# Kernel optimization log

Hardware: AMD Instinct MI355X
Metric: run time of the kernel (lower is better)

## Reference

```python
import jax, jax.numpy as jnp
import numpy as np

NUM_HEADS = 16

def setup_inputs() -> dict:
    key = jax.random.key(0)
    k1, k2, k3 = jax.random.split(key, 3)
    B, S, H = 2, 2048, 1024
    x = jax.random.normal(k1, (B, S, H), dtype=jnp.float32)
    w_qkv = jax.random.normal(k2, (H, 3 * H), dtype=jnp.float32) * (1.0 / np.sqrt(H))
    w_out = jax.random.normal(k3, (H, H), dtype=jnp.float32) * (1.0 / np.sqrt(H))
    return {"x": x, "w_qkv": w_qkv, "w_out": w_out}

def reference(x, w_qkv, w_out):
    B, S, H = x.shape
    nh = NUM_HEADS
    dh = H // nh
    qkv = x @ w_qkv  # (B, S, 3H)
    q, k, v = jnp.split(qkv, 3, axis=-1)
    # (B, nh, S, dh)
    q = q.reshape(B, S, nh, dh).transpose(0, 2, 1, 3)
    k = k.reshape(B, S, nh, dh).transpose(0, 2, 1, 3)
    v = v.reshape(B, S, nh, dh).transpose(0, 2, 1, 3)
    att = jnp.einsum('bhsd,bhSd->bhsS', q, k) / np.sqrt(dh).astype(np.float32)
    causal = jnp.tril(jnp.ones((S, S), dtype=bool))
    att = jnp.where(causal[None, None], att, -jnp.inf)
    att = jax.nn.softmax(att, axis=-1)
    out = jnp.einsum('bhsS,bhSd->bhsd', att, v)
    out = out.transpose(0, 2, 1, 3).reshape(B, S, H)
    return out @ w_out
```

## Files before the change

kernel.cpp:

```cpp
#include <hip/hip_runtime.h>

#define DEVINL __device__ __forceinline__

typedef __attribute__((ext_vector_type(8)))  __bf16         bf16x8;
typedef __attribute__((ext_vector_type(4)))  float          f32x4;
typedef __attribute__((ext_vector_type(16))) float          f32x16;
typedef __attribute__((ext_vector_type(8)))  unsigned short ushort8;
typedef __attribute__((ext_vector_type(4)))  unsigned short ushort4v;
typedef __attribute__((ext_vector_type(4)))  unsigned int   uint4v;
typedef __attribute__((ext_vector_type(4)))  float          float4v;

DEVINL unsigned short f2bf(float f) {
  unsigned int u = __float_as_uint(f);
  u += 0x7fffu + ((u >> 16) & 1u);
  return (unsigned short)(u >> 16);
}

DEVINL float bf2f(unsigned short u) {
  return __uint_as_float(((unsigned int)u) << 16);
}

DEVINL bf16x8 ldbf8(const unsigned short* p) {
  return __builtin_bit_cast(bf16x8, *(const ushort8*)p);
}

DEVINL unsigned cvtpk_bf16(float lo, float hi) {
  unsigned r;
  asm("v_cvt_pk_bf16_f32 %0, %1, %2" : "=v"(r) : "v"(lo), "v"(hi));
  return r;
}

DEVINL void gload_lds16(const unsigned short* g, unsigned short* l) {
  __builtin_amdgcn_global_load_lds((const __attribute__((address_space(1))) void*)g,
                                   (__attribute__((address_space(3))) void*)l, 16, 0, 0);
}

__global__ __launch_bounds__(256) void cvt_f32_bf16_kernel(
    const float* __restrict__ in, unsigned short* __restrict__ out, int n4) {
  int i = blockIdx.x * 256 + threadIdx.x;
  const int stride = gridDim.x * 256;
  for (; i < n4; i += stride) {
    float4v v = *(const float4v*)(in + (size_t)4 * i);
    ushort4v o;
    o[0] = f2bf(v[0]); o[1] = f2bf(v[1]); o[2] = f2bf(v[2]); o[3] = f2bf(v[3]);
    *(ushort4v*)(out + (size_t)4 * i) = o;
  }
}

__global__ __launch_bounds__(256) void transpose_cvt_kernel(
    const float* __restrict__ in, unsigned short* __restrict__ out, int R, int C) {
  __shared__ float tile[32][33];
  const int tx = threadIdx.x & 31, ty = threadIdx.x >> 5;
  const int r0 = blockIdx.y << 5, c0 = blockIdx.x << 5;
#pragma unroll
  for (int i = 0; i < 32; i += 8)
    tile[ty + i][tx] = in[(size_t)(r0 + ty + i) * C + (c0 + tx)];
  __syncthreads();
#pragma unroll
  for (int i = 0; i < 32; i += 8)
    out[(size_t)(c0 + ty + i) * R + (r0 + tx)] = f2bf(tile[tx][ty + i]);
}

template <bool OUT_BF16>
__global__ __launch_bounds__(256, 3) void gemm_bt_kernel(
    const unsigned short* __restrict__ A,
    const unsigned short* __restrict__ Bt,
    void* __restrict__ Cout,
    int M, int N, int K, int lda, int ldb, int ldc,
    unsigned short* __restrict__ VtOut) {
  __shared__ __align__(16) unsigned short As[2][128 * 32];
  __shared__ __align__(16) unsigned short Bs[2][128 * 32];
  const int tid = threadIdx.x;
  const int lane = tid & 63, wave = tid >> 6;
  const int wr = wave >> 1, wc = wave & 1;
  const int g = lane >> 4, q = lane & 15;
  const int row0 = blockIdx.x << 7, col0 = blockIdx.y << 7;

  const int srow = tid >> 2;
  const int sg = ((tid & 3) ^ (srow & 3)) << 3;
  const unsigned short* Ap0 = A + (size_t)(row0 + srow) * lda + sg;
  const unsigned short* Ap1 = Ap0 + (size_t)64 * lda;
  const unsigned short* Bp0 = Bt + (size_t)(col0 + srow) * ldb + sg;
  const unsigned short* Bp1 = Bp0 + (size_t)64 * ldb;

  f32x4 acc[4][4] = {};

  gload_lds16(Ap0, &As[0][wave * 512]);
  gload_lds16(Ap1, &As[0][2048 + wave * 512]);
  gload_lds16(Bp0, &Bs[0][wave * 512]);
  gload_lds16(Bp1, &Bs[0][2048 + wave * 512]);

  const int gx = (g ^ (q & 3)) << 3;
  const int nk = K >> 5;
  int cur = 0;

  for (int t = 0; t < nk; ++t) {
    if (t + 1 < nk) {
      Ap0 += 32; Ap1 += 32; Bp0 += 32; Bp1 += 32;
      gload_lds16(Ap0, &As[cur ^ 1][wave * 512]);
      gload_lds16(Ap1, &As[cur ^ 1][2048 + wave * 512]);
      gload_lds16(Bp0, &Bs[cur ^ 1][wave * 512]);
      gload_lds16(Bp1, &Bs[cur ^ 1][2048 + wave * 512]);
      asm volatile("s_waitcnt vmcnt(4)" ::: "memory");
    } else {
      asm volatile("s_waitcnt vmcnt(0)" ::: "memory");
    }
    __builtin_amdgcn_s_barrier();

    bf16x8 af[4], bfr[4];
#pragma unroll
    for (int mb = 0; mb < 4; ++mb)
      af[mb] = ldbf8(&As[cur][(wr * 64 + mb * 16 + q) * 32] + gx);
#pragma unroll
    for (int nb = 0; nb < 4; ++nb)
      bfr[nb] = ldbf8(&Bs[cur][(wc * 64 + nb * 16 + q) * 32] + gx);
#pragma unroll
    for (int mb = 0; mb < 4; ++mb)
#pragma unroll
      for (int nb = 0; nb < 4; ++nb)
        acc[mb][nb] = __builtin_amdgcn_mfma_f32_16x16x32_bf16(af[mb], bfr[nb], acc[mb][nb], 0, 0, 0);

    __builtin_amdgcn_s_barrier();
    cur ^= 1;
  }

  const bool isV = OUT_BF16 && (VtOut != nullptr) && (col0 >= 2048);
#pragma unroll
  for (int mb = 0; mb < 4; ++mb)
#pragma unroll
    for (int nb = 0; nb < 4; ++nb)
#pragma unroll
      for (int r = 0; r < 4; ++r) {
        const int row = row0 + wr * 64 + mb * 16 + g * 4 + r;
        const int col = col0 + wc * 64 + nb * 16 + q;
        const float v = acc[mb][nb][r];
        if (isV) {
          const int cp = col - 2048, hI = cp >> 6, dI = cp & 63;
          VtOut[((size_t)((row >> 11) * 16 + hI) * 64 + dI) * 2048 + (row & 2047)] = f2bf(v);
        } else if (OUT_BF16) {
          ((unsigned short*)Cout)[(size_t)row * ldc + col] = f2bf(v);
        } else {
          ((float*)Cout)[(size_t)row * ldc + col] = v;
        }
      }
}

__global__ __launch_bounds__(256, 2) void attn_kernel(
    const unsigned short* __restrict__ qkv,
    const unsigned short* __restrict__ VtG,
    unsigned short* __restrict__ OlP,
    unsigned short* __restrict__ OhP,
    float* __restrict__ stats) {
  const int S = 2048, H = 1024, LD = 2048;
  const int tid = threadIdx.x;
  const int wave = tid >> 6, lane = tid & 63;
  const int c = lane & 31, hh = lane >> 5;

  const int L = blockIdx.x;
  const int group = L >> 8, r0_ = L & 255;
  const int pairid = r0_ & 7, bh = r0_ >> 3;
  const int qc = (group & 2) ? (15 - pairid) : pairid;
  const int half = group & 1;
  const int b = bh >> 4, h = bh & 15;
  const int q0w = qc * 128 + wave * 32;

  const unsigned short* Qb = qkv + (size_t)b * S * LD + h * 64;
  const unsigned short* Kb = Qb + 1024;
  const unsigned short* Vt = VtG + (size_t)(b * 16 + h) * 64 * S;

  __shared__ __align__(16) unsigned short Ks[2][64 * 64];
  __shared__ __align__(16) unsigned short Vs[2][64 * 64];

  const int srow = lane >> 3;
  const int srcg = ((lane & 7) ^ srow) << 3;
  const int wrow = wave * 8 + srow;

  const int nit = qc + 1;
  const int tb = half ? nit : 0;

  {
    const int cc = tb << 6;
    gload_lds16(Kb + (size_t)(cc + wrow) * LD + srcg,      Ks[0] + wave * 512);
    gload_lds16(Kb + (size_t)(cc + 32 + wrow) * LD + srcg, Ks[0] + 2048 + wave * 512);
    gload_lds16(Vt + (size_t)wrow * S + cc + srcg,         Vs[0] + wave * 512);
    gload_lds16(Vt + (size_t)(32 + wrow) * S + cc + srcg,  Vs[0] + 2048 + wave * 512);
  }

  bf16x8 qf[4];
#pragma unroll
  for (int kc = 0; kc < 4; ++kc)
    qf[kc] = ldbf8(Qb + (size_t)(q0w + c) * LD + kc * 16 + hh * 8);

  f32x16 acc[2] = {};
  float m_r = -1e30f, l_r = 0.f;
  const float CE = 0.125f * 1.44269504f;

  int cur = 0;
  const int swz = (c & 7) << 3;

  for (int t = 0; t < nit; ++t) {
    if (t + 1 < nit) {
      const int c1 = (tb + t + 1) << 6;
      unsigned short* KsN = Ks[cur ^ 1];
      unsigned short* VsN = Vs[cur ^ 1];
      gload_lds16(Kb + (size_t)(c1 + wrow) * LD + srcg,      KsN + wave * 512);
      gload_lds16(Kb + (size_t)(c1 + 32 + wrow) * LD + srcg, KsN + 2048 + wave * 512);
      gload_lds16(Vt + (size_t)wrow * S + c1 + srcg,         VsN + wave * 512);
      gload_lds16(Vt + (size_t)(32 + wrow) * S + c1 + srcg,  VsN + 2048 + wave * 512);
      asm volatile("s_waitcnt vmcnt(4)" ::: "memory");
    } else {
      asm volatile("s_waitcnt vmcnt(0)" ::: "memory");
    }
    __builtin_amdgcn_s_barrier();

    const int c0 = (tb + t) << 6;
    const unsigned short* KsC = Ks[cur];
    const unsigned short* VsC = Vs[cur];

    if (c0 <= q0w + 31) {
      int nv = ((q0w + 31 - c0) >> 5) + 1; if (nv > 2) nv = 2;

      bf16x8 kf[2][4];
#pragma unroll
      for (int n = 0; n < 2; ++n) if (n < nv)
#pragma unroll
        for (int kc = 0; kc < 4; ++kc)
          kf[n][kc] = ldbf8(KsC + (n * 32 + c) * 64 + ((kc * 16 + hh * 8) ^ swz));

      f32x16 st[2] = {};
      __builtin_amdgcn_s_setprio(1);
#pragma unroll
      for (int n = 0; n < 2; ++n) if (n < nv)
#pragma unroll
        for (int kc = 0; kc < 4; ++kc)
          st[n] = __builtin_amdgcn_mfma_f32_32x32x16_bf16(kf[n][kc], qf[kc], st[n], 0, 0, 0);
      __builtin_amdgcn_s_setprio(0);

      bf16x8 vf[2][4];
#pragma unroll
      for (int db = 0; db < 2; ++db)
#pragma unroll
        for (int kk = 0; kk < 4; ++kk) if (kk < 2 * nv)
          vf[db][kk] = ldbf8(VsC + (db * 32 + c) * 64 + ((kk * 16 + hh * 8) ^ swz));

      if (c0 + 63 > q0w) {
#pragma unroll
        for (int n = 0; n < 2; ++n) if (n < nv)
#pragma unroll
          for (int r = 0; r < 16; ++r) {
            const int kv = c0 + n * 32 + (r & 3) + 8 * (r >> 2) + 4 * hh;
            if (kv > q0w + c) st[n][r] = -1e30f;
          }
      }

      float pmax = -1e30f;
#pragma unroll
      for (int n = 0; n < 2; ++n) if (n < nv)
#pragma unroll
        for (int r = 0; r < 16; ++r) pmax = fmaxf(pmax, st[n][r]);
      if (!__all(pmax <= m_r + 64.f)) {
        pmax = fmaxf(pmax, __shfl_xor(pmax, 32));
        const float mn = fmaxf(m_r, pmax);
        const float sf = __builtin_amdgcn_exp2f((m_r - mn) * CE);
        m_r = mn; l_r *= sf;
#pragma unroll
        for (int db = 0; db < 2; ++db) acc[db] *= sf;
      }
      const float mC = m_r * CE;
#pragma unroll
      for (int n = 0; n < 2; ++n) if (n < nv)
#pragma unroll
        for (int r = 0; r < 16; ++r) {
          const float p = __builtin_amdgcn_exp2f(fmaf(st[n][r], CE, -mC));
          st[n][r] = p;
          l_r += p;
        }

      bf16x8 pa[4];
#pragma unroll
      for (int n = 0; n < 2; ++n) if (n < nv) {
        unsigned T0 = cvtpk_bf16(st[n][0],  st[n][1]);
        unsigned T1 = cvtpk_bf16(st[n][2],  st[n][3]);
        unsigned T2 = cvtpk_bf16(st[n][4],  st[n][5]);
        unsigned T3 = cvtpk_bf16(st[n][6],  st[n][7]);
        unsigned T4 = cvtpk_bf16(st[n][8],  st[n][9]);
        unsigned T5 = cvtpk_bf16(st[n][10], st[n][11]);
        unsigned T6 = cvtpk_bf16(st[n][12], st[n][13]);
        unsigned T7 = cvtpk_bf16(st[n][14], st[n][15]);
        asm("v_permlane32_swap_b32 %0, %1" : "+v"(T0), "+v"(T2));
        asm("v_permlane32_swap_b32 %0, %1" : "+v"(T1), "+v"(T3));
        asm("v_permlane32_swap_b32 %0, %1" : "+v"(T4), "+v"(T6));
        asm("v_permlane32_swap_b32 %0, %1" : "+v"(T5), "+v"(T7));
        uint4v w0; w0[0] = T0; w0[1] = T1; w0[2] = T2; w0[3] = T3;
        uint4v w1; w1[0] = T4; w1[1] = T5; w1[2] = T6; w1[3] = T7;
        pa[2 * n]     = __builtin_bit_cast(bf16x8, w0);
        pa[2 * n + 1] = __builtin_bit_cast(bf16x8, w1);
      }

      __builtin_amdgcn_s_setprio(1);
#pragma unroll
      for (int kk = 0; kk < 4; ++kk) if (kk < 2 * nv)
#pragma unroll
        for (int db = 0; db < 2; ++db)
          acc[db] = __builtin_amdgcn_mfma_f32_32x32x16_bf16(vf[db][kk], pa[kk], acc[db], 0, 0, 0);
      __builtin_amdgcn_s_setprio(0);
    }

    __builtin_amdgcn_s_barrier();
    cur ^= 1;
  }

  const float lt = l_r + __shfl_xor(l_r, 32);
  const float inv = lt > 0.f ? 1.f / lt : 0.f;
  unsigned short* Op = half ? OhP : OlP;
  const size_t rowbase = (size_t)(b * S + q0w + c) * H + h * 64;
#pragma unroll
  for (int db = 0; db < 2; ++db)
#pragma unroll
    for (int blk = 0; blk < 4; ++blk) {
      ushort4v o;
#pragma unroll
      for (int j = 0; j < 4; ++j) o[j] = f2bf(acc[db][blk * 4 + j] * inv);
      *(ushort4v*)(Op + rowbase + db * 32 + blk * 8 + hh * 4) = o;
    }
  if (hh == 0) {
    float* sp = stats + ((((size_t)(b * 16 + h)) << 11) + q0w + c) * 4 + (half ? 2 : 0);
    sp[0] = m_r; sp[1] = lt;
  }
}

__global__ __launch_bounds__(256) void attn_merge_kernel(
    const unsigned short* __restrict__ Ol,
    const unsigned short* __restrict__ Oh,
    const float* __restrict__ stats,
    unsigned short* __restrict__ Oout) {
  const float CE = 0.125f * 1.44269504f;
  const int i = blockIdx.x * 256 + threadIdx.x;
  const int r = i >> 7;
  const int g8 = i & 127;
  const int h = g8 >> 3;
  const int s = r & 2047, b = r >> 11;
  const float4v st = *(const float4v*)(stats + ((((size_t)(b * 16 + h)) << 11) + s) * 4);
  const float mn = fmaxf(st[0], st[2]);
  const float wl_ = st[1] * __builtin_amdgcn_exp2f((st[0] - mn) * CE);
  const float wh_ = st[3] * __builtin_amdgcn_exp2f((st[2] - mn) * CE);
  const float inv = 1.f / (wl_ + wh_);
  const float wl = wl_ * inv, wh = wh_ * inv;
  const size_t off = (size_t)i * 8;
  const ushort8 a = *(const ushort8*)(Ol + off);
  const ushort8 cc = *(const ushort8*)(Oh + off);
  ushort8 o;
#pragma unroll
  for (int j = 0; j < 8; ++j)
    o[j] = f2bf(wl * bf2f(a[j]) + wh * bf2f(cc[j]));
  *(ushort8*)(Oout + off) = o;
}

extern "C" void kernel_launch(void* const* d_in, const int* in_sizes, int n_in,
                              void* d_out, int out_size, void* d_ws, size_t ws_size,
                              hipStream_t stream) {
  const float* x     = (const float*)d_in[0];
  const float* w_qkv = (const float*)d_in[1];
  const float* w_out = (const float*)d_in[2];
  const int B = 2, S = 2048, H = 1024;
  const int M = B * S;

  unsigned short* xb    = (unsigned short*)d_ws;
  unsigned short* wqkvT = xb + (size_t)M * H;
  unsigned short* woutT = wqkvT + (size_t)3 * H * H;
  unsigned short* qkb   = woutT + (size_t)H * H;
  unsigned short* VtG   = qkb + (size_t)M * 2048;
  unsigned short* Ob    = VtG + (size_t)B * 16 * 64 * S;
  unsigned short* OhP   = xb;
  float*          stats = (float*)wqkvT;

  cvt_f32_bf16_kernel<<<1024, 256, 0, stream>>>(x, xb, (M * H) / 4);
  transpose_cvt_kernel<<<dim3((3 * H) / 32, H / 32), 256, 0, stream>>>(w_qkv, wqkvT, H, 3 * H);
  transpose_cvt_kernel<<<dim3(H / 32, H / 32), 256, 0, stream>>>(w_out, woutT, H, H);

  gemm_bt_kernel<true><<<dim3(M / 128, (3 * H) / 128), 256, 0, stream>>>(
      xb, wqkvT, qkb, M, 3 * H, H, H, H, 2048, VtG);

  attn_kernel<<<1024, 256, 0, stream>>>(qkb, VtG, Ob, OhP, stats);

  attn_merge_kernel<<<2048, 256, 0, stream>>>(Ob, OhP, stats, Ob);

  gemm_bt_kernel<false><<<dim3(M / 128, H / 128), 256, 0, stream>>>(
      Ob, woutT, d_out, M, H, H, H, H, H, nullptr);
}
```

Before: 122.3 us.

## Split-K GEMM across two wave groups, fuse prepass kernels, split softmax reductions

Three unrelated changes. The three conversion/transpose kernels are merged into one prepass launch, removing two kernel launches. The GEMM now uses 512 threads with two wave groups, each handling half of K into its own LDS buffers, and the partial accumulators are reduced through LDS before the epilogue. This doubles waves per tile to hide latency, at the cost of extra LDS traffic and barriers. In attention, the row max and sum reductions use four independent accumulators to shorten the dependency chains.

```diff
diff --git a/kernel.cpp b/kernel.cpp
--- a/kernel.cpp
+++ b/kernel.cpp
@@ -35,23 +35,28 @@
                                    (__attribute__((address_space(3))) void*)l, 16, 0, 0);
 }
 
-__global__ __launch_bounds__(256) void cvt_f32_bf16_kernel(
-    const float* __restrict__ in, unsigned short* __restrict__ out, int n4) {
-  int i = blockIdx.x * 256 + threadIdx.x;
-  const int stride = gridDim.x * 256;
-  for (; i < n4; i += stride) {
-    float4v v = *(const float4v*)(in + (size_t)4 * i);
-    ushort4v o;
-    o[0] = f2bf(v[0]); o[1] = f2bf(v[1]); o[2] = f2bf(v[2]); o[3] = f2bf(v[3]);
-    *(ushort4v*)(out + (size_t)4 * i) = o;
-  }
-}
-
-__global__ __launch_bounds__(256) void transpose_cvt_kernel(
-    const float* __restrict__ in, unsigned short* __restrict__ out, int R, int C) {
+__global__ __launch_bounds__(256) void prepass_kernel(
+    const float* __restrict__ x, const float* __restrict__ w_qkv,
+    const float* __restrict__ w_out, unsigned short* __restrict__ xb,
+    unsigned short* __restrict__ wqkvT, unsigned short* __restrict__ woutT) {
   __shared__ float tile[32][33];
+  const int B = blockIdx.x;
+  if (B < 1024) {
+    const int n4 = 1048576;
+    for (int i = B * 256 + threadIdx.x; i < n4; i += 1024 * 256) {
+      float4v v = *(const float4v*)(x + (size_t)4 * i);
+      ushort4v o;
+      o[0] = f2bf(v[0]); o[1] = f2bf(v[1]); o[2] = f2bf(v[2]); o[3] = f2bf(v[3]);
+      *(ushort4v*)(xb + (size_t)4 * i) = o;
+    }
+    return;
+  }
+  const float* in; unsigned short* out; int C, bx, by;
+  if (B < 4096) { const int idx = B - 1024; bx = idx % 96; by = idx / 96; in = w_qkv; out = wqkvT; C = 3072; }
+  else          { const int idx = B - 4096; bx = idx & 31; by = idx >> 5; in = w_out; out = woutT; C = 1024; }
+  const int R = 1024;
   const int tx = threadIdx.x & 31, ty = threadIdx.x >> 5;
-  const int r0 = blockIdx.y << 5, c0 = blockIdx.x << 5;
+  const int r0 = by << 5, c0 = bx << 5;
 #pragma unroll
   for (int i = 0; i < 32; i += 8)
     tile[ty + i][tx] = in[(size_t)(r0 + ty + i) * C + (c0 + tx)];
@@ -62,45 +67,48 @@
 }
 
 template <bool OUT_BF16>
-__global__ __launch_bounds__(256, 3) void gemm_bt_kernel(
+__global__ __launch_bounds__(512, 2) void gemm_bt_kernel(
     const unsigned short* __restrict__ A,
     const unsigned short* __restrict__ Bt,
     void* __restrict__ Cout,
     int M, int N, int K, int lda, int ldb, int ldc,
     unsigned short* __restrict__ VtOut) {
-  __shared__ __align__(16) unsigned short As[2][128 * 32];
-  __shared__ __align__(16) unsigned short Bs[2][128 * 32];
+  __shared__ __align__(16) unsigned short As[2][2][128 * 32];
+  __shared__ __align__(16) unsigned short Bs[2][2][128 * 32];
   const int tid = threadIdx.x;
-  const int lane = tid & 63, wave = tid >> 6;
-  const int wr = wave >> 1, wc = wave & 1;
+  const int wave = tid >> 6, lane = tid & 63;
+  const int kg = wave >> 2, wsub = wave & 3;
+  const int wr = wsub >> 1, wc = wsub & 1;
   const int g = lane >> 4, q = lane & 15;
   const int row0 = blockIdx.x << 7, col0 = blockIdx.y << 7;
 
-  const int srow = tid >> 2;
-  const int sg = ((tid & 3) ^ (srow & 3)) << 3;
-  const unsigned short* Ap0 = A + (size_t)(row0 + srow) * lda + sg;
+  const int t = tid & 255;
+  const int srow = t >> 2;
+  const int sg = ((t & 3) ^ (srow & 3)) << 3;
+  const int K2 = K >> 1;
+  const unsigned short* Ap0 = A + (size_t)(row0 + srow) * lda + kg * K2 + sg;
   const unsigned short* Ap1 = Ap0 + (size_t)64 * lda;
-  const unsigned short* Bp0 = Bt + (size_t)(col0 + srow) * ldb + sg;
+  const unsigned short* Bp0 = Bt + (size_t)(col0 + srow) * ldb + kg * K2 + sg;
   const unsigned short* Bp1 = Bp0 + (size_t)64 * ldb;
 
   f32x4 acc[4][4] = {};
 
-  gload_lds16(Ap0, &As[0][wave * 512]);
-  gload_lds16(Ap1, &As[0][2048 + wave * 512]);
-  gload_lds16(Bp0, &Bs[0][wave * 512]);
-  gload_lds16(Bp1, &Bs[0][2048 + wave * 512]);
+  gload_lds16(Ap0, &As[kg][0][wsub * 512]);
+  gload_lds16(Ap1, &As[kg][0][2048 + wsub * 512]);
+  gload_lds16(Bp0, &Bs[kg][0][wsub * 512]);
+  gload_lds16(Bp1, &Bs[kg][0][2048 + wsub * 512]);
 
   const int gx = (g ^ (q & 3)) << 3;
-  const int nk = K >> 5;
+  const int nk = K2 >> 5;
   int cur = 0;
 
-  for (int t = 0; t < nk; ++t) {
-    if (t + 1 < nk) {
+  for (int it = 0; it < nk; ++it) {
+    if (it + 1 < nk) {
       Ap0 += 32; Ap1 += 32; Bp0 += 32; Bp1 += 32;
-      gload_lds16(Ap0, &As[cur ^ 1][wave * 512]);
-      gload_lds16(Ap1, &As[cur ^ 1][2048 + wave * 512]);
-      gload_lds16(Bp0, &Bs[cur ^ 1][wave * 512]);
-      gload_lds16(Bp1, &Bs[cur ^ 1][2048 + wave * 512]);
+      gload_lds16(Ap0, &As[kg][cur ^ 1][wsub * 512]);
+      gload_lds16(Ap1, &As[kg][cur ^ 1][2048 + wsub * 512]);
+      gload_lds16(Bp0, &Bs[kg][cur ^ 1][wsub * 512]);
+      gload_lds16(Bp1, &Bs[kg][cur ^ 1][2048 + wsub * 512]);
       asm volatile("s_waitcnt vmcnt(4)" ::: "memory");
     } else {
       asm volatile("s_waitcnt vmcnt(0)" ::: "memory");
@@ -110,10 +118,10 @@
     bf16x8 af[4], bfr[4];
 #pragma unroll
     for (int mb = 0; mb < 4; ++mb)
-      af[mb] = ldbf8(&As[cur][(wr * 64 + mb * 16 + q) * 32] + gx);
+      af[mb] = ldbf8(&As[kg][cur][(wr * 64 + mb * 16 + q) * 32] + gx);
 #pragma unroll
     for (int nb = 0; nb < 4; ++nb)
-      bfr[nb] = ldbf8(&Bs[cur][(wc * 64 + nb * 16 + q) * 32] + gx);
+      bfr[nb] = ldbf8(&Bs[kg][cur][(wc * 64 + nb * 16 + q) * 32] + gx);
 #pragma unroll
     for (int mb = 0; mb < 4; ++mb)
 #pragma unroll
@@ -124,25 +132,67 @@
     cur ^= 1;
   }
 
-  const bool isV = OUT_BF16 && (VtOut != nullptr) && (col0 >= 2048);
-#pragma unroll
-  for (int mb = 0; mb < 4; ++mb)
-#pragma unroll
-    for (int nb = 0; nb < 4; ++nb)
-#pragma unroll
-      for (int r = 0; r < 4; ++r) {
-        const int row = row0 + wr * 64 + mb * 16 + g * 4 + r;
-        const int col = col0 + wc * 64 + nb * 16 + q;
-        const float v = acc[mb][nb][r];
-        if (isV) {
-          const int cp = col - 2048, hI = cp >> 6, dI = cp & 63;
-          VtOut[((size_t)((row >> 11) * 16 + hI) * 64 + dI) * 2048 + (row & 2047)] = f2bf(v);
-        } else if (OUT_BF16) {
-          ((unsigned short*)Cout)[(size_t)row * ldc + col] = f2bf(v);
-        } else {
-          ((float*)Cout)[(size_t)row * ldc + col] = v;
+  float* mrg = (float*)&As[0][0][0];
+  __syncthreads();
+  if (kg == 1) {
+    float* p = mrg + t * 32;
+#pragma unroll
+    for (int mb = 0; mb < 2; ++mb)
+#pragma unroll
+      for (int nb = 0; nb < 4; ++nb)
+#pragma unroll
+        for (int r = 0; r < 4; ++r) p[mb * 16 + nb * 4 + r] = acc[mb][nb][r];
+  }
+  __syncthreads();
+  if (kg == 0) {
+    const float* p = mrg + t * 32;
+#pragma unroll
+    for (int mb = 0; mb < 2; ++mb)
+#pragma unroll
+      for (int nb = 0; nb < 4; ++nb)
+#pragma unroll
+        for (int r = 0; r < 4; ++r) acc[mb][nb][r] += p[mb * 16 + nb * 4 + r];
+  }
+  __syncthreads();
+  if (kg == 1) {
+    float* p = mrg + t * 32;
+#pragma unroll
+    for (int mb = 0; mb < 2; ++mb)
+#pragma unroll
+      for (int nb = 0; nb < 4; ++nb)
+#pragma unroll
+        for (int r = 0; r < 4; ++r) p[mb * 16 + nb * 4 + r] = acc[mb + 2][nb][r];
+  }
+  __syncthreads();
+  if (kg == 0) {
+    const float* p = mrg + t * 32;
+#pragma unroll
+    for (int mb = 0; mb < 2; ++mb)
+#pragma unroll
+      for (int nb = 0; nb < 4; ++nb)
+#pragma unroll
+        for (int r = 0; r < 4; ++r) acc[mb + 2][nb][r] += p[mb * 16 + nb * 4 + r];
+
+    const bool isV = OUT_BF16 && (VtOut != nullptr) && (col0 >= 2048);
+#pragma unroll
+    for (int mb = 0; mb < 4; ++mb)
+#pragma unroll
+      for (int nb = 0; nb < 4; ++nb)
+#pragma unroll
+        for (int r = 0; r < 4; ++r) {
+          const int row = row0 + wr * 64 + mb * 16 + g * 4 + r;
+          const int col = col0 + wc * 64 + nb * 16 + q;
+          const float v = acc[mb][nb][r];
+          if (isV) {
+            const int cp = col - 2048, hI = cp >> 6, dI = cp & 63;
+            VtOut[((size_t)((row >> 11) * 16 + hI) * 64 + dI) * 2048 + (row & 2047)] = f2bf(v);
+          } else if (OUT_BF16) {
+            ((unsigned short*)Cout)[(size_t)row * ldc + col] = f2bf(v);
+          } else {
+            ((float*)Cout)[(size_t)row * ldc + col] = v;
+          }
         }
-      }
+  }
 }
 
 __global__ __launch_bounds__(256, 2) void attn_kernel(
@@ -253,28 +303,31 @@
           }
       }
 
-      float pmax = -1e30f;
+      f32x4 pm = {-1e30f, -1e30f, -1e30f, -1e30f};
 #pragma unroll
       for (int n = 0; n < 2; ++n) if (n < nv)
 #pragma unroll
-        for (int r = 0; r < 16; ++r) pmax = fmaxf(pmax, st[n][r]);
+        for (int r = 0; r < 16; ++r) pm[r & 3] = fmaxf(pm[r & 3], st[n][r]);
+      const float pmax = fmaxf(fmaxf(pm[0], pm[1]), fmaxf(pm[2], pm[3]));
       if (!__all(pmax <= m_r + 64.f)) {
-        pmax = fmaxf(pmax, __shfl_xor(pmax, 32));
-        const float mn = fmaxf(m_r, pmax);
+        float px = fmaxf(pmax, __shfl_xor(pmax, 32));
+        const float mn = fmaxf(m_r, px);
         const float sf = __builtin_amdgcn_exp2f((m_r - mn) * CE);
         m_r = mn; l_r *= sf;
 #pragma unroll
         for (int db = 0; db < 2; ++db) acc[db] *= sf;
       }
       const float mC = m_r * CE;
+      f32x4 la = {0.f, 0.f, 0.f, 0.f};
 #pragma unroll
       for (int n = 0; n < 2; ++n) if (n < nv)
 #pragma unroll
         for (int r = 0; r < 16; ++r) {
           const float p = __builtin_amdgcn_exp2f(fmaf(st[n][r], CE, -mC));
           st[n][r] = p;
-          l_r += p;
+          la[r & 3] += p;
         }
+      l_r += (la[0] + la[1]) + (la[2] + la[3]);
 
       bf16x8 pa[4];
 #pragma unroll
@@ -374,17 +427,15 @@
   unsigned short* OhP   = xb;
   float*          stats = (float*)wqkvT;
 
-  cvt_f32_bf16_kernel<<<1024, 256, 0, stream>>>(x, xb, (M * H) / 4);
-  transpose_cvt_kernel<<<dim3((3 * H) / 32, H / 32), 256, 0, stream>>>(w_qkv, wqkvT, H, 3 * H);
-  transpose_cvt_kernel<<<dim3(H / 32, H / 32), 256, 0, stream>>>(w_out, woutT, H, H);
-
-  gemm_bt_kernel<true><<<dim3(M / 128, (3 * H) / 128), 256, 0, stream>>>(
+  prepass_kernel<<<5120, 256, 0, stream>>>(x, w_qkv, w_out, xb, wqkvT, woutT);
+
+  gemm_bt_kernel<true><<<dim3(M / 128, (3 * H) / 128), 512, 0, stream>>>(
       xb, wqkvT, qkb, M, 3 * H, H, H, H, 2048, VtG);
 
   attn_kernel<<<1024, 256, 0, stream>>>(qkb, VtG, Ob, OhP, stats);
 
   attn_merge_kernel<<<2048, 256, 0, stream>>>(Ob, OhP, stats, Ob);
 
-  gemm_bt_kernel<false><<<dim3(M / 128, H / 128), 256, 0, stream>>>(
+  gemm_bt_kernel<false><<<dim3(M / 128, H / 128), 512, 0, stream>>>(
       Ob, woutT, d_out, M, H, H, H, H, H, nullptr);
 }
```

New measurement: 131.8 us. +7.7%, slower.

## Fuse prepass kernels, add 64-row output GEMM, split softmax reductions

Applied to the files above, without the earlier changes.

Merges the three conversion/transpose launches into one prepass kernel that dispatches on block index, cutting launch overhead. Adds a 64x128-tile GEMM for the output projection, doubling its grid (512 blocks) to fill more CUs on a small problem. In the attention softmax, the row max and row sum now use four independent partial accumulators, which shortens dependency chains. The smaller GEMM tile lowers data reuse per block, and the four-way partial sum slightly changes the floating-point summation order.

```diff
diff --git a/kernel.cpp b/kernel.cpp
--- a/kernel.cpp
+++ b/kernel.cpp
@@ -35,23 +35,28 @@
                                    (__attribute__((address_space(3))) void*)l, 16, 0, 0);
 }
 
-__global__ __launch_bounds__(256) void cvt_f32_bf16_kernel(
-    const float* __restrict__ in, unsigned short* __restrict__ out, int n4) {
-  int i = blockIdx.x * 256 + threadIdx.x;
-  const int stride = gridDim.x * 256;
-  for (; i < n4; i += stride) {
-    float4v v = *(const float4v*)(in + (size_t)4 * i);
-    ushort4v o;
-    o[0] = f2bf(v[0]); o[1] = f2bf(v[1]); o[2] = f2bf(v[2]); o[3] = f2bf(v[3]);
-    *(ushort4v*)(out + (size_t)4 * i) = o;
-  }
-}
-
-__global__ __launch_bounds__(256) void transpose_cvt_kernel(
-    const float* __restrict__ in, unsigned short* __restrict__ out, int R, int C) {
+__global__ __launch_bounds__(256) void prepass_kernel(
+    const float* __restrict__ x, const float* __restrict__ w_qkv,
+    const float* __restrict__ w_out, unsigned short* __restrict__ xb,
+    unsigned short* __restrict__ wqkvT, unsigned short* __restrict__ woutT) {
   __shared__ float tile[32][33];
+  const int B = blockIdx.x;
+  if (B < 1024) {
+    const int n4 = 1048576;
+    for (int i = B * 256 + threadIdx.x; i < n4; i += 1024 * 256) {
+      float4v v = *(const float4v*)(x + (size_t)4 * i);
+      ushort4v o;
+      o[0] = f2bf(v[0]); o[1] = f2bf(v[1]); o[2] = f2bf(v[2]); o[3] = f2bf(v[3]);
+      *(ushort4v*)(xb + (size_t)4 * i) = o;
+    }
+    return;
+  }
+  const float* in; unsigned short* out; int C, bx, by;
+  if (B < 4096) { const int idx = B - 1024; bx = idx % 96; by = idx / 96; in = w_qkv; out = wqkvT; C = 3072; }
+  else          { const int idx = B - 4096; bx = idx & 31; by = idx >> 5; in = w_out; out = woutT; C = 1024; }
+  const int R = 1024;
   const int tx = threadIdx.x & 31, ty = threadIdx.x >> 5;
-  const int r0 = blockIdx.y << 5, c0 = blockIdx.x << 5;
+  const int r0 = by << 5, c0 = bx << 5;
 #pragma unroll
   for (int i = 0; i < 32; i += 8)
     tile[ty + i][tx] = in[(size_t)(r0 + ty + i) * C + (c0 + tx)];
@@ -145,6 +150,76 @@
       }
 }
 
+__global__ __launch_bounds__(256, 3) void gemm_bt64_kernel(
+    const unsigned short* __restrict__ A,
+    const unsigned short* __restrict__ Bt,
+    float* __restrict__ Cout,
+    int K, int lda, int ldb, int ldc) {
+  __shared__ __align__(16) unsigned short As[2][64 * 32];
+  __shared__ __align__(16) unsigned short Bs[2][128 * 32];
+  const int tid = threadIdx.x;
+  const int lane = tid & 63, wave = tid >> 6;
+  const int wr = wave >> 1, wc = wave & 1;
+  const int g = lane >> 4, q = lane & 15;
+  const int row0 = blockIdx.x << 6, col0 = blockIdx.y << 7;
+
+  const int srow = tid >> 2;
+  const int sg = ((tid & 3) ^ (srow & 3)) << 3;
+  const unsigned short* Ap = A + (size_t)(row0 + srow) * lda + sg;
+  const unsigned short* Bp0 = Bt + (size_t)(col0 + srow) * ldb + sg;
+  const unsigned short* Bp1 = Bp0 + (size_t)64 * ldb;
+
+  f32x4 acc[2][4] = {};
+
+  gload_lds16(Ap, &As[0][wave * 512]);
+  gload_lds16(Bp0, &Bs[0][wave * 512]);
+  gload_lds16(Bp1, &Bs[0][2048 + wave * 512]);
+
+  const int gx = (g ^ (q & 3)) << 3;
+  const int nk = K >> 5;
+  int cur = 0;
+
+  for (int t = 0; t < nk; ++t) {
+    if (t + 1 < nk) {
+      Ap += 32; Bp0 += 32; Bp1 += 32;
+      gload_lds16(Ap, &As[cur ^ 1][wave * 512]);
+      gload_lds16(Bp0, &Bs[cur ^ 1][wave * 512]);
+      gload_lds16(Bp1, &Bs[cur ^ 1][2048 + wave * 512]);
+      asm volatile("s_waitcnt vmcnt(3)" ::: "memory");
+    } else {
+      asm volatile("s_waitcnt vmcnt(0)" ::: "memory");
+    }
+    __builtin_amdgcn_s_barrier();
+
+    bf16x8 af[2], bfr[4];
+#pragma unroll
+    for (int mb = 0; mb < 2; ++mb)
+      af[mb] = ldbf8(&As[cur][(wr * 32 + mb * 16 + q) * 32] + gx);
+#pragma unroll
+    for (int nb = 0; nb < 4; ++nb)
+      bfr[nb] = ldbf8(&Bs[cur][(wc * 64 + nb * 16 + q) * 32] + gx);
+#pragma unroll
+    for (int mb = 0; mb < 2; ++mb)
+#pragma unroll
+      for (int nb = 0; nb < 4; ++nb)
+        acc[mb][nb] = __builtin_amdgcn_mfma_f32_16x16x32_bf16(af[mb], bfr[nb], acc[mb][nb], 0, 0, 0);
+
+    __builtin_amdgcn_s_barrier();
+    cur ^= 1;
+  }
+
+#pragma unroll
+  for (int mb = 0; mb < 2; ++mb)
+#pragma unroll
+    for (int nb = 0; nb < 4; ++nb)
+#pragma unroll
+      for (int r = 0; r < 4; ++r) {
+        const int row = row0 + wr * 32 + mb * 16 + g * 4 + r;
+        const int col = col0 + wc * 64 + nb * 16 + q;
+        Cout[(size_t)row * ldc + col] = acc[mb][nb][r];
+      }
+}
+
 __global__ __launch_bounds__(256, 2) void attn_kernel(
     const unsigned short* __restrict__ qkv,
     const unsigned short* __restrict__ VtG,
@@ -253,28 +328,31 @@
           }
       }
 
-      float pmax = -1e30f;
+      f32x4 pm = {-1e30f, -1e30f, -1e30f, -1e30f};
 #pragma unroll
       for (int n = 0; n < 2; ++n) if (n < nv)
 #pragma unroll
-        for (int r = 0; r < 16; ++r) pmax = fmaxf(pmax, st[n][r]);
+        for (int r = 0; r < 16; ++r) pm[r & 3] = fmaxf(pm[r & 3], st[n][r]);
+      const float pmax = fmaxf(fmaxf(pm[0], pm[1]), fmaxf(pm[2], pm[3]));
       if (!__all(pmax <= m_r + 64.f)) {
-        pmax = fmaxf(pmax, __shfl_xor(pmax, 32));
-        const float mn = fmaxf(m_r, pmax);
+        float px = fmaxf(pmax, __shfl_xor(pmax, 32));
+        const float mn = fmaxf(m_r, px);
         const float sf = __builtin_amdgcn_exp2f((m_r - mn) * CE);
         m_r = mn; l_r *= sf;
 #pragma unroll
         for (int db = 0; db < 2; ++db) acc[db] *= sf;
       }
       const float mC = m_r * CE;
+      f32x4 la = {0.f, 0.f, 0.f, 0.f};
 #pragma unroll
       for (int n = 0; n < 2; ++n) if (n < nv)
 #pragma unroll
         for (int r = 0; r < 16; ++r) {
           const float p = __builtin_amdgcn_exp2f(fmaf(st[n][r], CE, -mC));
           st[n][r] = p;
-          l_r += p;
+          la[r & 3] += p;
         }
+      l_r += (la[0] + la[1]) + (la[2] + la[3]);
 
       bf16x8 pa[4];
 #pragma unroll
@@ -374,9 +452,7 @@
   unsigned short* OhP   = xb;
   float*          stats = (float*)wqkvT;
 
-  cvt_f32_bf16_kernel<<<1024, 256, 0, stream>>>(x, xb, (M * H) / 4);
-  transpose_cvt_kernel<<<dim3((3 * H) / 32, H / 32), 256, 0, stream>>>(w_qkv, wqkvT, H, 3 * H);
-  transpose_cvt_kernel<<<dim3(H / 32, H / 32), 256, 0, stream>>>(w_out, woutT, H, H);
+  prepass_kernel<<<5120, 256, 0, stream>>>(x, w_qkv, w_out, xb, wqkvT, woutT);
 
   gemm_bt_kernel<true><<<dim3(M / 128, (3 * H) / 128), 256, 0, stream>>>(
       xb, wqkvT, qkb, M, 3 * H, H, H, H, 2048, VtG);
@@ -385,6 +461,6 @@
 
   attn_merge_kernel<<<2048, 256, 0, stream>>>(Ob, OhP, stats, Ob);
 
-  gemm_bt_kernel<false><<<dim3(M / 128, H / 128), 256, 0, stream>>>(
-      Ob, woutT, d_out, M, H, H, H, H, H, nullptr);
-}
+  gemm_bt64_kernel<<<dim3(M / 64, H / 128), 256, 0, stream>>>(
+      Ob, woutT, (float*)d_out, H, H, H, H);
+}
```

New measurement: 116.6 us, median of 2. 1.05x faster.
